# Kernel tuning notes

Hardware: AMD Instinct MI355X
Metric: run time of the kernel (lower is better)

The kernel has to match this reference:

```python
import jax, jax.numpy as jnp
import numpy as np

B, P, C = 64, 8732, 81
NEG_POS_RATIO = 3


def _smooth_l1_masked_sum(p, t, maskf):
    # smooth_l1 with beta=1, sum reduction, restricted to positive priors
    d = jnp.abs(p - t)
    l = jnp.where(d < 1.0, 0.5 * d * d, d - 0.5)  # [B,P,K]
    return jnp.sum(l.sum(-1) * maskf)


def setup_inputs() -> dict:
    key = jax.random.key(0)
    ks = jax.random.split(key, 6)
    loc_data = jax.random.normal(ks[0], (B, P, 4), jnp.float32)
    conf_data = jax.random.normal(ks[1], (B, P, C), jnp.float32)
    four_corners_data = jax.random.normal(ks[2], (B, P, 8), jnp.float32)
    loc_t = jax.random.normal(ks[3], (B, P, 4), jnp.float32)
    four_corners_t = jax.random.normal(ks[4], (B, P, 8), jnp.float32)
    conf_t = jax.random.randint(ks[5], (B, P), 0, C, jnp.int32)
    return {
        "loc_data": loc_data,
        "conf_data": conf_data,
        "four_corners_data": four_corners_data,
        "loc_t": loc_t,
        "four_corners_t": four_corners_t,
        "conf_t": conf_t,
    }


def reference(loc_data, conf_data, four_corners_data, loc_t, four_corners_t, conf_t):
    num_priors = conf_data.shape[1]
    pos = conf_t > 0                                  # [B,P]
    posf = pos.astype(conf_data.dtype)

    # localization + four-corner smooth-L1 over matched (positive) priors
    loss_l = _smooth_l1_masked_sum(loc_data, loc_t, posf)
    loss_four_corners = _smooth_l1_masked_sum(four_corners_data, four_corners_t, posf)

    # per-prior CE loss: log_sum_exp(conf) - conf[target]
    lse = jax.nn.logsumexp(conf_data, axis=-1)        # [B,P]
    gathered = jnp.take_along_axis(conf_data, conf_t[..., None], axis=-1)[..., 0]
    ce_all = lse - gathered                           # [B,P]

    # hard-negative mining: rank negatives by CE loss (double argsort)
    loss_c_mine = jnp.where(pos, 0.0, ce_all)
    loss_idx = jnp.argsort(-loss_c_mine, axis=1)      # descending sort indices
    idx_rank = jnp.argsort(loss_idx, axis=1)          # rank of each prior
    num_pos = pos.sum(axis=1, keepdims=True)          # [B,1]
    num_neg = jnp.minimum(NEG_POS_RATIO * num_pos, num_priors - 1)
    neg = idx_rank < num_neg                          # [B,P]

    sel = pos | neg
    loss_c = jnp.sum(jnp.where(sel, ce_all, 0.0))

    N = num_pos.sum().astype(conf_data.dtype)
    return (loss_l / N, loss_c / N, loss_four_corners / N)
```

## Files before the change

### kernel.cpp

```cpp
#include <hip/hip_runtime.h>


#define NB 64
#define NP 8732
#define NC 81
constexpr int BP = NB * NP;
constexpr int PBLK = (NP + 255) / 256;

__device__ inline float sl1(float d) {
    d = fabsf(d);
    return d < 1.0f ? 0.5f * d * d : d - 0.5f;
}

__global__ void k_init(float* acc_area) {
    if (threadIdx.x < 194) acc_area[threadIdx.x] = 0.0f;
}

__global__ __launch_bounds__(256) void k_main(
    const float* __restrict__ loc_data, const float* __restrict__ conf_data,
    const float* __restrict__ fc_data,  const float* __restrict__ loc_t,
    const float* __restrict__ fc_t,     const int* __restrict__ conf_t,
    float* __restrict__ ce, float* __restrict__ acc,
    int* __restrict__ npos_b, float* __restrict__ spos_b, float* __restrict__ sneg_b)
{
    const int b = blockIdx.y;
    const int t = threadIdx.x;
    const int p = (blockIdx.x << 8) + t;

    float l_sum = 0.0f, f_sum = 0.0f, sp = 0.0f, sn = 0.0f;
    int np = 0;

    if (p < NP) {
        const size_t g = (size_t)b * NP + p;
        const int tgt = conf_t[g];
        const float posf = (tgt > 0) ? 1.0f : 0.0f;
        np = (tgt > 0) ? 1 : 0;

        float4 a  = ((const float4*)loc_data)[g];
        float4 at = ((const float4*)loc_t)[g];
        l_sum = (sl1(a.x - at.x) + sl1(a.y - at.y) +
                 sl1(a.z - at.z) + sl1(a.w - at.w)) * posf;
        float4 c0 = ((const float4*)fc_data)[2 * g];
        float4 c1 = ((const float4*)fc_data)[2 * g + 1];
        float4 d0 = ((const float4*)fc_t)[2 * g];
        float4 d1 = ((const float4*)fc_t)[2 * g + 1];
        f_sum = (sl1(c0.x - d0.x) + sl1(c0.y - d0.y) + sl1(c0.z - d0.z) + sl1(c0.w - d0.w) +
                 sl1(c1.x - d1.x) + sl1(c1.y - d1.y) + sl1(c1.z - d1.z) + sl1(c1.w - d1.w)) * posf;

        const float* row = conf_data + g * NC;
        float s0 = 0.0f, s1 = 0.0f, s2 = 0.0f, s3 = 0.0f;
        #pragma unroll 5
        for (int c = 0; c < 80; c += 4) {
            s0 += __expf(row[c]);
            s1 += __expf(row[c + 1]);
            s2 += __expf(row[c + 2]);
            s3 += __expf(row[c + 3]);
        }
        float s = (s0 + s1) + (s2 + s3) + __expf(row[80]);
        float cev = __logf(s) - row[tgt];
        ce[g] = cev;
        sp = cev * posf;
        sn = cev - sp;
    }

    __shared__ float red[4][5];
    const int wave = t >> 6, lane = t & 63;
    float vnp = (float)np;
    #pragma unroll
    for (int o = 32; o; o >>= 1) {
        l_sum += __shfl_xor(l_sum, o, 64);
        f_sum += __shfl_xor(f_sum, o, 64);
        sp    += __shfl_xor(sp, o, 64);
        sn    += __shfl_xor(sn, o, 64);
        vnp   += __shfl_xor(vnp, o, 64);
    }
    if (lane == 0) {
        red[wave][0] = l_sum; red[wave][1] = f_sum;
        red[wave][2] = sp;    red[wave][3] = sn;   red[wave][4] = vnp;
    }
    __syncthreads();
    if (t == 0) {
        float rl = 0, rf = 0, rp = 0, rn = 0, rc = 0;
        #pragma unroll
        for (int w = 0; w < 4; ++w) {
            rl += red[w][0]; rf += red[w][1]; rp += red[w][2];
            rn += red[w][3]; rc += red[w][4];
        }
        atomicAdd(&acc[0], rl);
        atomicAdd(&acc[1], rf);
        atomicAdd(&spos_b[b], rp);
        atomicAdd(&sneg_b[b], rn);
        atomicAdd(&npos_b[b], (int)rc);
    }
}

__global__ __launch_bounds__(256) void k_batch(
    const float* __restrict__ ce, const int* __restrict__ conf_t,
    const int* __restrict__ npos_b, const float* __restrict__ spos_b,
    const float* __restrict__ sneg_b, float* __restrict__ loss_c_b)
{
    const int b = blockIdx.x;
    const int t = threadIdx.x;
    const int npos    = npos_b[b];
    const int nneg    = NP - npos;
    const int num_neg = min(3 * npos, NP - 1);

    if (num_neg >= nneg) {
        if (t == 0) loss_c_b[b] = spos_b[b] + sneg_b[b];
        return;
    }
    if (num_neg <= 0) {
        if (t == 0) loss_c_b[b] = spos_b[b];
        return;
    }

    __shared__ float ce_s[NP];
    __shared__ float sredf[4];
    __shared__ int   sredi[4];
    const float* crow = ce + (size_t)b * NP;
    const int*   trow = conf_t + (size_t)b * NP;
    for (int p = t; p < NP; p += 256)
        ce_s[p] = (trow[p] > 0) ? -1.0f : crow[p];
    __syncthreads();

    const int wave = t >> 6, lane = t & 63;
    const int K = num_neg;
    unsigned lo = 0u, hi = 0x7f800000u;
    while (lo < hi) {
        unsigned mid = lo + ((hi - lo) >> 1);
        float v = __uint_as_float(mid);
        int c_t = 0;
        for (int p = t; p < NP; p += 256) c_t += (ce_s[p] > v) ? 1 : 0;
        #pragma unroll
        for (int o = 32; o; o >>= 1) c_t += __shfl_xor(c_t, o, 64);
        __syncthreads();
        if (lane == 0) sredi[wave] = c_t;
        __syncthreads();
        int cnt = sredi[0] + sredi[1] + sredi[2] + sredi[3];
        if (cnt < K) hi = mid; else lo = mid + 1;
    }
    float v = __uint_as_float(lo);
    int c_t = 0; float s_t = 0.0f;
    for (int p = t; p < NP; p += 256) {
        float x = ce_s[p];
        if (x > v) { c_t++; s_t += x; }
    }
    #pragma unroll
    for (int o = 32; o; o >>= 1) {
        c_t += __shfl_xor(c_t, o, 64);
        s_t += __shfl_xor(s_t, o, 64);
    }
    __syncthreads();
    if (lane == 0) { sredi[wave] = c_t; sredf[wave] = s_t; }
    __syncthreads();
    if (t == 0) {
        int   cnt = sredi[0] + sredi[1] + sredi[2] + sredi[3];
        float sgt = sredf[0] + sredf[1] + sredf[2] + sredf[3];
        loss_c_b[b] = spos_b[b] + sgt + (float)(K - cnt) * v;
    }
}

__global__ void k_final(const float* __restrict__ acc,
                        const float* __restrict__ loss_c_b,
                        const int* __restrict__ npos_b,
                        float* __restrict__ out)
{
    const int t = threadIdx.x;
    float lc = loss_c_b[t];
    int   np = npos_b[t];
    #pragma unroll
    for (int o = 32; o; o >>= 1) {
        lc += __shfl_xor(lc, o, 64);
        np += __shfl_xor(np, o, 64);
    }
    if (t == 0) {
        float N = (float)np;
        out[0] = acc[0] / N;
        out[1] = lc / N;
        out[2] = acc[1] / N;
    }
}

extern "C" void kernel_launch(void* const* d_in, const int* in_sizes, int n_in,
                              void* d_out, int out_size, void* d_ws, size_t ws_size,
                              hipStream_t stream)
{
    const float* loc_data  = (const float*)d_in[0];
    const float* conf_data = (const float*)d_in[1];
    const float* fc_data   = (const float*)d_in[2];
    const float* loc_t     = (const float*)d_in[3];
    const float* fc_t      = (const float*)d_in[4];
    const int*   conf_t    = (const int*)d_in[5];
    float* out = (float*)d_out;

    float* ce       = (float*)d_ws;
    float* acc      = ce + BP;
    int*   npos_b   = (int*)(acc + 2);
    float* spos_b   = (float*)(npos_b + 64);
    float* sneg_b   = spos_b + 64;
    float* loss_c_b = sneg_b + 64;

    hipLaunchKernelGGL(k_init,  dim3(1), dim3(256), 0, stream, acc);
    hipLaunchKernelGGL(k_main,  dim3(PBLK, NB), dim3(256), 0, stream,
                       loc_data, conf_data, fc_data, loc_t, fc_t, conf_t,
                       ce, acc, npos_b, spos_b, sneg_b);
    hipLaunchKernelGGL(k_batch, dim3(NB), dim3(256), 0, stream,
                       ce, conf_t, npos_b, spos_b, sneg_b, loss_c_b);
    hipLaunchKernelGGL(k_final, dim3(1), dim3(64), 0, stream,
                       acc, loss_c_b, npos_b, out);
}
```

Baseline: 315.6 us.

## Stage conf rows through LDS with coalesced float4 loads and 4 lanes per row

Replaces the per-thread strided walk over each 81-float conf row with a cooperative, coalesced float4 copy of 64 rows at a time into shared memory. Four lanes then compute each row's exp-sum and combine with shuffles. This targets the uncoalesced global access pattern of the old logsumexp loop, at the cost of extra LDS traffic and block-wide syncs per 64-row chunk.

Result: slower. 339.0 us (+7.4%).

```diff
diff --git a/kernel.cpp b/kernel.cpp
--- a/kernel.cpp
+++ b/kernel.cpp
@@ -23,47 +23,82 @@
     float* __restrict__ ce, float* __restrict__ acc,
     int* __restrict__ npos_b, float* __restrict__ spos_b, float* __restrict__ sneg_b)
 {
-    const int b = blockIdx.y;
-    const int t = threadIdx.x;
-    const int p = (blockIdx.x << 8) + t;
+    const int b  = blockIdx.y;
+    const int t  = threadIdx.x;
+    const int p0 = blockIdx.x << 8;
+    const int nrows = min(256, NP - p0);
+
+    __shared__ __align__(16) float tile[64 * NC + 4];
+    __shared__ int   tgt_s[256];
+    __shared__ float red[4][5];
 
     float l_sum = 0.0f, f_sum = 0.0f, sp = 0.0f, sn = 0.0f;
     int np = 0;
 
-    if (p < NP) {
-        const size_t g = (size_t)b * NP + p;
-        const int tgt = conf_t[g];
-        const float posf = (tgt > 0) ? 1.0f : 0.0f;
-        np = (tgt > 0) ? 1 : 0;
-
-        float4 a  = ((const float4*)loc_data)[g];
-        float4 at = ((const float4*)loc_t)[g];
-        l_sum = (sl1(a.x - at.x) + sl1(a.y - at.y) +
-                 sl1(a.z - at.z) + sl1(a.w - at.w)) * posf;
-        float4 c0 = ((const float4*)fc_data)[2 * g];
-        float4 c1 = ((const float4*)fc_data)[2 * g + 1];
-        float4 d0 = ((const float4*)fc_t)[2 * g];
-        float4 d1 = ((const float4*)fc_t)[2 * g + 1];
-        f_sum = (sl1(c0.x - d0.x) + sl1(c0.y - d0.y) + sl1(c0.z - d0.z) + sl1(c0.w - d0.w) +
-                 sl1(c1.x - d1.x) + sl1(c1.y - d1.y) + sl1(c1.z - d1.z) + sl1(c1.w - d1.w)) * posf;
-
-        const float* row = conf_data + g * NC;
-        float s0 = 0.0f, s1 = 0.0f, s2 = 0.0f, s3 = 0.0f;
-        #pragma unroll 5
-        for (int c = 0; c < 80; c += 4) {
-            s0 += __expf(row[c]);
-            s1 += __expf(row[c + 1]);
-            s2 += __expf(row[c + 2]);
-            s3 += __expf(row[c + 3]);
+    {
+        const int p = p0 + t;
+        int tgt = 0;
+        if (p < NP) {
+            const size_t g = (size_t)b * NP + p;
+            tgt = conf_t[g];
+            const float posf = (tgt > 0) ? 1.0f : 0.0f;
+            np = (tgt > 0) ? 1 : 0;
+            float4 a4  = ((const float4*)loc_data)[g];
+            float4 a4t = ((const float4*)loc_t)[g];
+            l_sum = (sl1(a4.x - a4t.x) + sl1(a4.y - a4t.y) +
+                     sl1(a4.z - a4t.z) + sl1(a4.w - a4t.w)) * posf;
+            float4 c0 = ((const float4*)fc_data)[2 * g];
+            float4 c1 = ((const float4*)fc_data)[2 * g + 1];
+            float4 d0 = ((const float4*)fc_t)[2 * g];
+            float4 d1 = ((const float4*)fc_t)[2 * g + 1];
+            f_sum = (sl1(c0.x - d0.x) + sl1(c0.y - d0.y) + sl1(c0.z - d0.z) + sl1(c0.w - d0.w) +
+                     sl1(c1.x - d1.x) + sl1(c1.y - d1.y) + sl1(c1.z - d1.z) + sl1(c1.w - d1.w)) * posf;
         }
-        float s = (s0 + s1) + (s2 + s3) + __expf(row[80]);
-        float cev = __logf(s) - row[tgt];
-        ce[g] = cev;
-        sp = cev * posf;
-        sn = cev - sp;
-    }
-
-    __shared__ float red[4][5];
+        tgt_s[t] = tgt;
+    }
+
+    const size_t gbase = ((size_t)b * NP + p0) * (size_t)NC;
+    const int al = (int)(gbase & 3);
+    const float* conf_al = conf_data + (gbase - (size_t)al);
+    const int r = t >> 2, sub = t & 3;
+
+    for (int s = 0; s < 4; ++s) {
+        const int r0 = s << 6;
+        const int rs = min(64, nrows - r0);
+        if (rs <= 0) break;
+        const int nf  = al + rs * NC;
+        const int n4  = nf >> 2;
+        const int rem = nf & 3;
+
+        __syncthreads();
+        const float4* src4 = (const float4*)(conf_al + (size_t)r0 * NC);
+        float4* dst4 = (float4*)tile;
+        for (int j = t; j < n4; j += 256) dst4[j] = src4[j];
+        if (t < rem) tile[(n4 << 2) + t] = conf_al[(size_t)r0 * NC + (n4 << 2) + t];
+        __syncthreads();
+
+        if (r < rs) {
+            const float* lrow = tile + al + r * NC;
+            float s0 = 0.0f, s1 = 0.0f;
+            int c = sub;
+            #pragma unroll
+            for (int k = 0; k < 10; ++k) {
+                s0 += __expf(lrow[c]); c += 4;
+                s1 += __expf(lrow[c]); c += 4;
+            }
+            if (sub == 0) s0 += __expf(lrow[80]);
+            float ss = s0 + s1;
+            ss += __shfl_xor(ss, 1, 64);
+            ss += __shfl_xor(ss, 2, 64);
+            if (sub == 0) {
+                const int tgt = tgt_s[r0 + r];
+                const float cev = __logf(ss) - lrow[tgt];
+                ce[(size_t)b * NP + (size_t)(p0 + r0 + r)] = cev;
+                if (tgt > 0) sp += cev; else sn += cev;
+            }
+        }
+    }
+
     const int wave = t >> 6, lane = t & 63;
     float vnp = (float)np;
     #pragma unroll
```
